# Performance work log

Measured on AMD Instinct MI355X. Metric: run time of the kernel, lower is better.

The kernel has to match this reference:

```python
import jax, jax.numpy as jnp
import numpy as np

N, E = 100000, 1000000          # nodes, edges
IN, OUT = 64, 64                # feature dims
R, B = 16, 8                    # num_rels, num_bases


def setup_inputs() -> dict:
    key = jax.random.key(0)
    k = jax.random.split(key, 6)
    h = jax.random.normal(k[0], (N, IN), jnp.float32)
    weight = jax.random.normal(k[1], (B, IN, OUT), jnp.float32) * 0.05
    w_comp = jax.random.normal(k[2], (R, B), jnp.float32) * 0.3
    src = jax.random.randint(k[3], (E,), 0, N, jnp.int32)
    dst = jax.random.randint(k[4], (E,), 0, N, jnp.int32)
    rel = jax.random.randint(k[5], (E,), 0, R, jnp.int32)
    return {"h": h, "weight": weight, "w_comp": w_comp,
            "src": src, "dst": dst, "rel": rel}


def _rel_weights(weight, w_comp):
    # Faithful replication of the torch basis-combination including its
    # exact (reinterpreting) view calls:
    #   weight.view(in, B, out); matmul(w_comp, .); .view(R, in, out)
    V = weight.reshape(IN, B, OUT)                 # reinterpret, not transpose
    M = jnp.einsum('rb,ibo->iro', w_comp, V)       # [IN, R, OUT]
    return M.reshape(R, IN, OUT)


def reference(h, weight, w_comp, src, dst, rel):
    W = _rel_weights(weight, w_comp)               # [R, IN, OUT]
    # msg_e = h[src_e] @ W[rel_e]; computed without materializing [E,IN,OUT]:
    proj = jnp.einsum('nd,rdf->nrf', h, W)         # [N, R, OUT]
    msg = proj[src, rel]                           # [E, OUT] per-edge gather
    h2 = jax.ops.segment_sum(msg, dst, num_segments=N)  # fn.sum -> 'h2'
    # apply_func: bias is None (falsy); returns activation(old h).
    # Note: original apply_func reads but does not use h2 (tutorial quirk);
    # we return both the updated 'h' and the aggregated 'h2'.
    h_new = jax.nn.relu(h)
    return h_new, h2
```

## Files before the change

kernel.cpp:

```cpp
#include <hip/hip_runtime.h>
#include <hip/hip_bf16.h>

#define NN 100000
#define EE 1000000
#define FDIM 64
#define NREL 16
#define NBASE 8
#define HN (NN * FDIM)
#define H4 (HN / 4)
#define WSZ (NREL * FDIM * FDIM)
#define NPAD 100032
#define PCOLS 1024
#define NB_SCAN ((NN + 255) / 256)
#define EGX 128

typedef __attribute__((ext_vector_type(8))) short short8;
typedef __attribute__((ext_vector_type(4))) float f32x4;

static __device__ __forceinline__ ushort f2bf(float f) {
    __hip_bfloat16 b = __float2bfloat16(f);
    return *(ushort*)&b;
}
static __device__ __forceinline__ float bf2f(ushort u) {
    unsigned x = ((unsigned)u) << 16;
    float f;
    __builtin_memcpy(&f, &x, 4);
    return f;
}

__global__ void prep_kernel(const float4* __restrict__ h4, float4* __restrict__ out4,
                            ushort2* __restrict__ hb2,
                            const float* __restrict__ weight,
                            const float* __restrict__ w_comp, ushort* __restrict__ WT,
                            int* __restrict__ cnt, int czn,
                            float4* __restrict__ h2z, int zero_h2) {
    int gid = blockIdx.x * blockDim.x + threadIdx.x;
    if (gid < czn) cnt[gid] = 0;
    if (gid < WSZ) {
        int r = gid >> 12;
        int o = (gid >> 6) & 63;
        int d = gid & 63;
        const float* wc = w_comp + (d & 15) * NBASE;
        const float* wv = weight + (size_t)(4 * r + (d >> 4)) * 512 + o;
        float acc = 0.f;
#pragma unroll
        for (int b = 0; b < NBASE; ++b)
            acc = fmaf(wc[b], wv[b * 64], acc);
        WT[gid] = f2bf(acc);
    }
    if (gid < H4) {
        float4 v = h4[gid];
        ushort2 lo, hi;
        lo.x = f2bf(v.x); lo.y = f2bf(v.y);
        hi.x = f2bf(v.z); hi.y = f2bf(v.w);
        hb2[2 * gid] = lo;
        hb2[2 * gid + 1] = hi;
        v.x = fmaxf(v.x, 0.f); v.y = fmaxf(v.y, 0.f);
        v.z = fmaxf(v.z, 0.f); v.w = fmaxf(v.w, 0.f);
        out4[gid] = v;
        if (zero_h2) h2z[gid] = make_float4(0.f, 0.f, 0.f, 0.f);
    }
}


__global__ __launch_bounds__(256) void proj_gemm_kernel(
    const ushort* __restrict__ hb, const ushort* __restrict__ WT,
    ushort* __restrict__ projb, const int* __restrict__ dst, int* __restrict__ cnt) {
    const int wv = threadIdx.x >> 6;
    const int lane = threadIdx.x & 63;
    const int quad = lane >> 4, l15 = lane & 15;
    const int row0 = blockIdx.x * 64;
    const int col0 = blockIdx.y * 256 + wv * 64;

    if (blockIdx.y == 0) {
        int tid = blockIdx.x * 256 + threadIdx.x;
        int stride = gridDim.x * 256;
        for (int i = tid; i < EE; i += stride)
            atomicAdd(&cnt[dst[i]], 1);
    }

    short8 Af[4][2];
#pragma unroll
    for (int g = 0; g < 4; ++g) {
        const short8* ar = (const short8*)(hb + (size_t)(row0 + 16 * g + l15) * 64);
        Af[g][0] = ar[quad];
        Af[g][1] = ar[4 + quad];
    }
    short8 Bf[2][4];
#pragma unroll
    for (int t = 0; t < 4; ++t) {
        const short8* br = (const short8*)(WT + (size_t)(col0 + 16 * t + l15) * 64);
        Bf[0][t] = br[quad];
        Bf[1][t] = br[4 + quad];
    }
    f32x4 acc[4][4];
#pragma unroll
    for (int g = 0; g < 4; ++g)
#pragma unroll
        for (int t = 0; t < 4; ++t) acc[g][t] = (f32x4){0.f, 0.f, 0.f, 0.f};
#pragma unroll
    for (int g = 0; g < 4; ++g)
#pragma unroll
        for (int t = 0; t < 4; ++t) {
            acc[g][t] = __builtin_amdgcn_mfma_f32_16x16x32_bf16(Af[g][0], Bf[0][t], acc[g][t], 0, 0, 0);
            acc[g][t] = __builtin_amdgcn_mfma_f32_16x16x32_bf16(Af[g][1], Bf[1][t], acc[g][t], 0, 0, 0);
        }
#pragma unroll
    for (int g = 0; g < 4; ++g) {
        int rbase = row0 + 16 * g + quad * 4;
#pragma unroll
        for (int t = 0; t < 4; ++t) {
            size_t cb = (size_t)(col0 + 16 * t + l15);
#pragma unroll
            for (int r = 0; r < 4; ++r)
                projb[(size_t)(rbase + r) * PCOLS + cb] = f2bf(acc[g][t][r]);
        }
    }
}

__global__ __launch_bounds__(256) void scan_a_kernel(const int* __restrict__ cnt,
                                                     int* __restrict__ bsum) {
    int i = blockIdx.x * 256 + threadIdx.x;
    int v = (i < NN) ? cnt[i] : 0;
#pragma unroll
    for (int o = 32; o > 0; o >>= 1) v += __shfl_down(v, o, 64);
    __shared__ int ws4[4];
    if ((threadIdx.x & 63) == 0) ws4[threadIdx.x >> 6] = v;
    __syncthreads();
    if (threadIdx.x == 0) bsum[blockIdx.x] = ws4[0] + ws4[1] + ws4[2] + ws4[3];
}

__global__ __launch_bounds__(512) void scan_b_kernel(const int* __restrict__ bsum,
                                                     int* __restrict__ bbase,
                                                     int* __restrict__ off) {
    __shared__ int lds[512];
    int t = threadIdx.x;
    int v = (t < NB_SCAN) ? bsum[t] : 0;
    lds[t] = v;
    __syncthreads();
    for (int o = 1; o < 512; o <<= 1) {
        int u = (t >= o) ? lds[t - o] : 0;
        __syncthreads();
        lds[t] += u;
        __syncthreads();
    }
    if (t < NB_SCAN) bbase[t] = lds[t] - v;
    if (t == NB_SCAN - 1) off[NN] = lds[t];
}

__global__ __launch_bounds__(256) void scan_c_kernel(const int* __restrict__ cnt,
                                                     const int* __restrict__ bbase,
                                                     int* __restrict__ off,
                                                     int* __restrict__ cur) {
    __shared__ int lds[256];
    int i = blockIdx.x * 256 + threadIdx.x;
    int t = threadIdx.x;
    int v = (i < NN) ? cnt[i] : 0;
    lds[t] = v;
    __syncthreads();
    for (int o = 1; o < 256; o <<= 1) {
        int u = (t >= o) ? lds[t - o] : 0;
        __syncthreads();
        lds[t] += u;
        __syncthreads();
    }
    if (i < NN) {
        int excl = lds[t] - v + bbase[blockIdx.x];
        off[i] = excl;
        cur[i] = excl;
    }
}

__global__ void scatter_dst_kernel(const int* __restrict__ src, const int* __restrict__ dst,
                                   const int* __restrict__ rel, int* __restrict__ cur,
                                   int* __restrict__ pidx) {
    int i = blockIdx.x * blockDim.x + threadIdx.x;
    if (i < EE) {
        int pos = atomicAdd(&cur[dst[i]], 1);
        pidx[pos] = src[i] * 16 + rel[i];
    }
}

__global__ __launch_bounds__(256) void aggregate_kernel(
    const int* __restrict__ off, const int* __restrict__ pidx,
    const ushort* __restrict__ projb, float* __restrict__ h2) {
    int wv = (blockIdx.x * 256 + threadIdx.x) >> 6;
    int lane = threadIdx.x & 63;
    int v = __builtin_amdgcn_readfirstlane(wv);
    if (v >= NN) return;
    int s = off[v], e = off[v + 1];
    float acc = 0.f;
    int i = s;
    for (; i + 4 <= e; i += 4) {
        int p0 = pidx[i], p1 = pidx[i + 1], p2 = pidx[i + 2], p3 = pidx[i + 3];
        float a = bf2f(projb[(size_t)p0 * 64 + lane]);
        float b = bf2f(projb[(size_t)p1 * 64 + lane]);
        float c = bf2f(projb[(size_t)p2 * 64 + lane]);
        float d = bf2f(projb[(size_t)p3 * 64 + lane]);
        acc += (a + b) + (c + d);
    }
    for (; i < e; ++i)
        acc += bf2f(projb[(size_t)pidx[i] * 64 + lane]);
    h2[(size_t)v * 64 + lane] = acc;
}


__global__ void hist16_kernel(const int* __restrict__ rel, int* __restrict__ counts) {
    __shared__ int lc[NREL];
    if (threadIdx.x < NREL) lc[threadIdx.x] = 0;
    __syncthreads();
    int stride = gridDim.x * blockDim.x;
    for (int i = blockIdx.x * blockDim.x + threadIdx.x; i < EE; i += stride)
        atomicAdd(&lc[rel[i]], 1);
    __syncthreads();
    if (threadIdx.x < NREL && lc[threadIdx.x] > 0)
        atomicAdd(&counts[threadIdx.x], lc[threadIdx.x]);
}

__global__ void scan16_kernel(const int* __restrict__ counts,
                              int* __restrict__ offsets, int* __restrict__ cursors) {
    if (threadIdx.x == 0 && blockIdx.x == 0) {
        int acc = 0;
        for (int r = 0; r < NREL; ++r) { offsets[r] = acc; cursors[r] = acc; acc += counts[r]; }
        offsets[NREL] = acc;
    }
}

__global__ void scatter16_kernel(const int* __restrict__ rel, const int* __restrict__ src,
                                 const int* __restrict__ dst, int* __restrict__ cursors,
                                 int* __restrict__ src_bin, int* __restrict__ dst_bin) {
    __shared__ int lhist[NREL];
    __shared__ int lbase[NREL];
    int i = blockIdx.x * blockDim.x + threadIdx.x;
    if (threadIdx.x < NREL) lhist[threadIdx.x] = 0;
    __syncthreads();
    int r = 0, rank = 0;
    if (i < EE) { r = rel[i]; rank = atomicAdd(&lhist[r], 1); }
    __syncthreads();
    if (threadIdx.x < NREL && lhist[threadIdx.x] > 0)
        lbase[threadIdx.x] = atomicAdd(&cursors[threadIdx.x], lhist[threadIdx.x]);
    __syncthreads();
    if (i < EE) {
        int pos = lbase[r] + rank;
        src_bin[pos] = src[i];
        dst_bin[pos] = dst[i];
    }
}

__global__ __launch_bounds__(256) void edge_mfma_kernel(
    const int* __restrict__ offsets, const int* __restrict__ src_bin,
    const int* __restrict__ dst_bin, const ushort* __restrict__ hb,
    const ushort* __restrict__ WT, float* __restrict__ h2) {
    const int rel = blockIdx.y;
    const int lane = threadIdx.x & 63;
    const int quad = lane >> 4;
    const int l15 = lane & 15;
    const int start = offsets[rel];
    const int end = offsets[rel + 1];
    const int cnt = end - start;
    if (cnt <= 0) return;

    const short8* wt = (const short8*)(WT + rel * 4096);
    short8 Bf[2][4];
#pragma unroll
    for (int t = 0; t < 4; ++t) {
#pragma unroll
        for (int s = 0; s < 2; ++s)
            Bf[s][t] = wt[((t * 16 + l15) << 3) + (s << 2) + quad];
    }
    const int nw = EGX * 4;
    const int wave = blockIdx.x * 4 + (threadIdx.x >> 6);
    const int nb = (cnt + 15) >> 4;
    const int per = (nb + nw - 1) / nw;
    int b0 = wave * per;
    int b1 = b0 + per; if (b1 > nb) b1 = nb;
    const int quad4 = quad * 4;

    for (int b = b0; b < b1; ++b) {
        const int base = start + (b << 4);
        int ei = base + l15; if (ei >= end) ei = end - 1;
        int s0 = src_bin[ei];
        const short8* ar = (const short8*)(hb + (size_t)s0 * FDIM);
        short8 A0 = ar[quad];
        short8 A1 = ar[4 + quad];
        f32x4 acc[4];
#pragma unroll
        for (int t = 0; t < 4; ++t) acc[t] = (f32x4){0.f, 0.f, 0.f, 0.f};
#pragma unroll
        for (int t = 0; t < 4; ++t) {
            acc[t] = __builtin_amdgcn_mfma_f32_16x16x32_bf16(A0, Bf[0][t], acc[t], 0, 0, 0);
            acc[t] = __builtin_amdgcn_mfma_f32_16x16x32_bf16(A1, Bf[1][t], acc[t], 0, 0, 0);
        }
#pragma unroll
        for (int r = 0; r < 4; ++r) {
            int em = base + quad4 + r;
            if (em < end) {
                int dv = dst_bin[em];
                float* p = h2 + (size_t)dv * FDIM + l15;
                unsafeAtomicAdd(p,      acc[0][r]);
                unsafeAtomicAdd(p + 16, acc[1][r]);
                unsafeAtomicAdd(p + 32, acc[2][r]);
                unsafeAtomicAdd(p + 48, acc[3][r]);
            }
        }
    }
}

extern "C" void kernel_launch(void* const* d_in, const int* in_sizes, int n_in,
                              void* d_out, int out_size, void* d_ws, size_t ws_size,
                              hipStream_t stream) {
    const float* h      = (const float*)d_in[0];
    const float* weight = (const float*)d_in[1];
    const float* w_comp = (const float*)d_in[2];
    const int*   src    = (const int*)d_in[3];
    const int*   dst    = (const int*)d_in[4];
    const int*   rel    = (const int*)d_in[5];

    float* out_hnew = (float*)d_out;
    float* out_h2   = out_hnew + HN;

    char* ws = (char*)d_ws;

    size_t o_cnt  = 131072;
    size_t o_off  = o_cnt + 400000;
    size_t o_cur  = o_off + 400016;
    size_t o_pidx = o_cur + 400000;
    size_t o_bsum = o_pidx + 4000000;
    size_t o_bbas = o_bsum + 4 * ((NB_SCAN + 3) & ~3);
    size_t o_hb   = o_bbas + 4 * ((NB_SCAN + 3) & ~3);
    size_t o_proj = o_hb + (size_t)NPAD * 128;
    size_t need   = o_proj + (size_t)NPAD * 2048;

    if (ws_size >= need) {
        ushort* WT    = (ushort*)ws;
        int*    cnt   = (int*)(ws + o_cnt);
        int*    off   = (int*)(ws + o_off);
        int*    cur   = (int*)(ws + o_cur);
        int*    pidx  = (int*)(ws + o_pidx);
        int*    bsum  = (int*)(ws + o_bsum);
        int*    bbase = (int*)(ws + o_bbas);
        ushort* hb    = (ushort*)(ws + o_hb);
        ushort* projb = (ushort*)(ws + o_proj);

        hipLaunchKernelGGL(prep_kernel, dim3((H4 + 255) / 256), dim3(256), 0, stream,
                           (const float4*)h, (float4*)out_hnew, (ushort2*)hb,
                           weight, w_comp, WT, cnt, NN, (float4*)out_h2, 0);
        hipLaunchKernelGGL(proj_gemm_kernel, dim3(NPAD / 64, 4), dim3(256), 0, stream,
                           hb, WT, projb, dst, cnt);
        hipLaunchKernelGGL(scan_a_kernel, dim3(NB_SCAN), dim3(256), 0, stream, cnt, bsum);
        hipLaunchKernelGGL(scan_b_kernel, dim3(1), dim3(512), 0, stream, bsum, bbase, off);
        hipLaunchKernelGGL(scan_c_kernel, dim3(NB_SCAN), dim3(256), 0, stream,
                           cnt, bbase, off, cur);
        hipLaunchKernelGGL(scatter_dst_kernel, dim3((EE + 255) / 256), dim3(256), 0, stream,
                           src, dst, rel, cur, pidx);
        hipLaunchKernelGGL(aggregate_kernel, dim3(NN / 4), dim3(256), 0, stream,
                           off, pidx, projb, out_h2);
    } else {
        ushort* WT      = (ushort*)ws;
        int*    meta    = (int*)(ws + 0x20000);
        int*    counts  = meta;
        int*    offsets = meta + 16;
        int*    cursors = meta + 33;
        int*    src_bin = (int*)(ws + 0x20400);
        int*    dst_bin = (int*)(ws + 0x20400 + 4 * EE);
        ushort* hb      = (ushort*)(ws + 0x20400 + 8 * EE);

        hipLaunchKernelGGL(prep_kernel, dim3((H4 + 255) / 256), dim3(256), 0, stream,
                           (const float4*)h, (float4*)out_hnew, (ushort2*)hb,
                           weight, w_comp, WT, counts, 16, (float4*)out_h2, 1);
        hipLaunchKernelGGL(hist16_kernel, dim3(1024), dim3(256), 0, stream, rel, counts);
        hipLaunchKernelGGL(scan16_kernel, dim3(1), dim3(64), 0, stream,
                           counts, offsets, cursors);
        hipLaunchKernelGGL(scatter16_kernel, dim3((EE + 255) / 256), dim3(256), 0, stream,
                           rel, src, dst, cursors, src_bin, dst_bin);
        hipLaunchKernelGGL(edge_mfma_kernel, dim3(EGX, NREL), dim3(256), 0, stream,
                           offsets, src_bin, dst_bin, hb, WT, out_h2);
    }
}
```

Baseline: 324.3 us.

## Fuse scan stages and scatter+aggregate into persistent kernels with grid barriers

```diff
diff --git a/kernel.cpp b/kernel.cpp
--- a/kernel.cpp
+++ b/kernel.cpp
@@ -11,7 +11,9 @@
 #define WSZ (NREL * FDIM * FDIM)
 #define NPAD 100032
 #define PCOLS 1024
-#define NB_SCAN ((NN + 255) / 256)
+#define SB 512
+#define NBLK ((NN + SB - 1) / SB)
+#define SAB 512
 #define EGX 128
 
 typedef __attribute__((ext_vector_type(8))) short short8;
@@ -79,129 +81,148 @@
             atomicAdd(&cnt[dst[i]], 1);
     }
 
-    short8 Af[4][2];
+    short8 Wf[4][2];
+#pragma unroll
+    for (int ct = 0; ct < 4; ++ct) {
+        const short8* wr = (const short8*)(WT + (size_t)(col0 + 16 * ct + l15) * 64);
+        Wf[ct][0] = wr[quad];
+        Wf[ct][1] = wr[4 + quad];
+    }
+    short8 Hf[4][2];
 #pragma unroll
     for (int g = 0; g < 4; ++g) {
-        const short8* ar = (const short8*)(hb + (size_t)(row0 + 16 * g + l15) * 64);
-        Af[g][0] = ar[quad];
-        Af[g][1] = ar[4 + quad];
-    }
-    short8 Bf[2][4];
-#pragma unroll
-    for (int t = 0; t < 4; ++t) {
-        const short8* br = (const short8*)(WT + (size_t)(col0 + 16 * t + l15) * 64);
-        Bf[0][t] = br[quad];
-        Bf[1][t] = br[4 + quad];
+        const short8* hr = (const short8*)(hb + (size_t)(row0 + 16 * g + l15) * 64);
+        Hf[g][0] = hr[quad];
+        Hf[g][1] = hr[4 + quad];
     }
     f32x4 acc[4][4];
 #pragma unroll
-    for (int g = 0; g < 4; ++g)
-#pragma unroll
-        for (int t = 0; t < 4; ++t) acc[g][t] = (f32x4){0.f, 0.f, 0.f, 0.f};
-#pragma unroll
-    for (int g = 0; g < 4; ++g)
-#pragma unroll
-        for (int t = 0; t < 4; ++t) {
-            acc[g][t] = __builtin_amdgcn_mfma_f32_16x16x32_bf16(Af[g][0], Bf[0][t], acc[g][t], 0, 0, 0);
-            acc[g][t] = __builtin_amdgcn_mfma_f32_16x16x32_bf16(Af[g][1], Bf[1][t], acc[g][t], 0, 0, 0);
+    for (int ct = 0; ct < 4; ++ct)
+#pragma unroll
+        for (int g = 0; g < 4; ++g) acc[ct][g] = (f32x4){0.f, 0.f, 0.f, 0.f};
+#pragma unroll
+    for (int ct = 0; ct < 4; ++ct)
+#pragma unroll
+        for (int g = 0; g < 4; ++g) {
+            acc[ct][g] = __builtin_amdgcn_mfma_f32_16x16x32_bf16(Wf[ct][0], Hf[g][0], acc[ct][g], 0, 0, 0);
+            acc[ct][g] = __builtin_amdgcn_mfma_f32_16x16x32_bf16(Wf[ct][1], Hf[g][1], acc[ct][g], 0, 0, 0);
         }
 #pragma unroll
     for (int g = 0; g < 4; ++g) {
-        int rbase = row0 + 16 * g + quad * 4;
-#pragma unroll
-        for (int t = 0; t < 4; ++t) {
-            size_t cb = (size_t)(col0 + 16 * t + l15);
-#pragma unroll
-            for (int r = 0; r < 4; ++r)
-                projb[(size_t)(rbase + r) * PCOLS + cb] = f2bf(acc[g][t][r]);
-        }
-    }
-}
-
-__global__ __launch_bounds__(256) void scan_a_kernel(const int* __restrict__ cnt,
-                                                     int* __restrict__ bsum) {
-    int i = blockIdx.x * 256 + threadIdx.x;
+        size_t nrow = (size_t)(row0 + 16 * g + l15) * PCOLS;
+#pragma unroll
+        for (int ct = 0; ct < 4; ++ct) {
+            int c = col0 + 16 * ct + quad * 4;
+            unsigned u0 = ((unsigned)f2bf(acc[ct][g][1]) << 16) | f2bf(acc[ct][g][0]);
+            unsigned u1 = ((unsigned)f2bf(acc[ct][g][3]) << 16) | f2bf(acc[ct][g][2]);
+            *(uint2*)(projb + nrow + c) = make_uint2(u0, u1);
+        }
+    }
+}
+
+__global__ __launch_bounds__(SB) void scan_fused_kernel(
+    const int* __restrict__ cnt, int* __restrict__ off, int* __restrict__ cur,
+    int* __restrict__ bsum, int* __restrict__ bbase, int* __restrict__ sync) {
+    __shared__ int lds[SB];
+    __shared__ int lastBlk;
+    const int b = blockIdx.x, t = threadIdx.x;
+    const int i = b * SB + t;
     int v = (i < NN) ? cnt[i] : 0;
-#pragma unroll
-    for (int o = 32; o > 0; o >>= 1) v += __shfl_down(v, o, 64);
-    __shared__ int ws4[4];
-    if ((threadIdx.x & 63) == 0) ws4[threadIdx.x >> 6] = v;
-    __syncthreads();
-    if (threadIdx.x == 0) bsum[blockIdx.x] = ws4[0] + ws4[1] + ws4[2] + ws4[3];
-}
-
-__global__ __launch_bounds__(512) void scan_b_kernel(const int* __restrict__ bsum,
-                                                     int* __restrict__ bbase,
-                                                     int* __restrict__ off) {
-    __shared__ int lds[512];
-    int t = threadIdx.x;
-    int v = (t < NB_SCAN) ? bsum[t] : 0;
     lds[t] = v;
     __syncthreads();
-    for (int o = 1; o < 512; o <<= 1) {
+    for (int o = 1; o < SB; o <<= 1) {
         int u = (t >= o) ? lds[t - o] : 0;
         __syncthreads();
         lds[t] += u;
         __syncthreads();
     }
-    if (t < NB_SCAN) bbase[t] = lds[t] - v;
-    if (t == NB_SCAN - 1) off[NN] = lds[t];
-}
-
-__global__ __launch_bounds__(256) void scan_c_kernel(const int* __restrict__ cnt,
-                                                     const int* __restrict__ bbase,
-                                                     int* __restrict__ off,
-                                                     int* __restrict__ cur) {
-    __shared__ int lds[256];
-    int i = blockIdx.x * 256 + threadIdx.x;
-    int t = threadIdx.x;
-    int v = (i < NN) ? cnt[i] : 0;
-    lds[t] = v;
-    __syncthreads();
-    for (int o = 1; o < 256; o <<= 1) {
-        int u = (t >= o) ? lds[t - o] : 0;
+    int incl = lds[t];
+    if (t == SB - 1) bsum[b] = incl;
+    __threadfence();
+    __syncthreads();
+    if (t == 0) {
+        int prev = __hip_atomic_fetch_add(&sync[0], 1, __ATOMIC_ACQ_REL, __HIP_MEMORY_SCOPE_AGENT);
+        lastBlk = (prev == gridDim.x - 1);
+    }
+    __syncthreads();
+    if (lastBlk) {
+        __shared__ int lds2[256];
+        int vb = 0;
+        if (t < 256) {
+            vb = (t < NBLK) ? __hip_atomic_load(&bsum[t], __ATOMIC_RELAXED, __HIP_MEMORY_SCOPE_AGENT) : 0;
+            lds2[t] = vb;
+        }
         __syncthreads();
-        lds[t] += u;
+        for (int o = 1; o < 256; o <<= 1) {
+            int u = (t >= o && t < 256) ? lds2[t - o] : 0;
+            __syncthreads();
+            if (t < 256) lds2[t] += u;
+            __syncthreads();
+        }
+        if (t < NBLK) bbase[t] = lds2[t] - vb;
+        if (t == NBLK - 1) off[NN] = lds2[t];
+        __threadfence();
         __syncthreads();
-    }
+        if (t == 0)
+            __hip_atomic_store(&sync[1], 1, __ATOMIC_RELEASE, __HIP_MEMORY_SCOPE_AGENT);
+    }
+    if (t == 0) {
+        while (__hip_atomic_load(&sync[1], __ATOMIC_ACQUIRE, __HIP_MEMORY_SCOPE_AGENT) == 0)
+            __builtin_amdgcn_s_sleep(8);
+    }
+    __syncthreads();
+    int base = __hip_atomic_load(&bbase[b], __ATOMIC_RELAXED, __HIP_MEMORY_SCOPE_AGENT);
     if (i < NN) {
-        int excl = lds[t] - v + bbase[blockIdx.x];
+        int excl = incl - v + base;
         off[i] = excl;
         cur[i] = excl;
     }
 }
 
-__global__ void scatter_dst_kernel(const int* __restrict__ src, const int* __restrict__ dst,
-                                   const int* __restrict__ rel, int* __restrict__ cur,
-                                   int* __restrict__ pidx) {
-    int i = blockIdx.x * blockDim.x + threadIdx.x;
-    if (i < EE) {
+__global__ __launch_bounds__(256) void scatter_agg_kernel(
+    const int* __restrict__ src, const int* __restrict__ dst,
+    const int* __restrict__ rel, int* __restrict__ cur, int* __restrict__ pidx,
+    const int* __restrict__ off, const ushort* __restrict__ projb,
+    float* __restrict__ h2, int* __restrict__ sync) {
+    int tid = blockIdx.x * 256 + threadIdx.x;
+    int stride = SAB * 256;
+    for (int i = tid; i < EE; i += stride) {
         int pos = atomicAdd(&cur[dst[i]], 1);
         pidx[pos] = src[i] * 16 + rel[i];
     }
-}
-
-__global__ __launch_bounds__(256) void aggregate_kernel(
-    const int* __restrict__ off, const int* __restrict__ pidx,
-    const ushort* __restrict__ projb, float* __restrict__ h2) {
-    int wv = (blockIdx.x * 256 + threadIdx.x) >> 6;
-    int lane = threadIdx.x & 63;
-    int v = __builtin_amdgcn_readfirstlane(wv);
-    if (v >= NN) return;
-    int s = off[v], e = off[v + 1];
-    float acc = 0.f;
-    int i = s;
-    for (; i + 4 <= e; i += 4) {
-        int p0 = pidx[i], p1 = pidx[i + 1], p2 = pidx[i + 2], p3 = pidx[i + 3];
-        float a = bf2f(projb[(size_t)p0 * 64 + lane]);
-        float b = bf2f(projb[(size_t)p1 * 64 + lane]);
-        float c = bf2f(projb[(size_t)p2 * 64 + lane]);
-        float d = bf2f(projb[(size_t)p3 * 64 + lane]);
-        acc += (a + b) + (c + d);
-    }
-    for (; i < e; ++i)
-        acc += bf2f(projb[(size_t)pidx[i] * 64 + lane]);
-    h2[(size_t)v * 64 + lane] = acc;
+    __threadfence();
+    __syncthreads();
+    if (threadIdx.x == 0) {
+        __hip_atomic_fetch_add(&sync[2], 1, __ATOMIC_ACQ_REL, __HIP_MEMORY_SCOPE_AGENT);
+        while (__hip_atomic_load(&sync[2], __ATOMIC_ACQUIRE, __HIP_MEMORY_SCOPE_AGENT) < SAB)
+            __builtin_amdgcn_s_sleep(8);
+    }
+    __syncthreads();
+
+    const int lane = threadIdx.x & 63;
+    const int w = tid >> 6;
+    const int nwv = SAB * 4;
+    for (int v = w; v < NN; v += nwv) {
+        int s = off[v], e = off[v + 1];
+        float acc = 0.f;
+        int i = s;
+        for (; i + 4 <= e; i += 4) {
+            int p0 = __hip_atomic_load(&pidx[i],     __ATOMIC_RELAXED, __HIP_MEMORY_SCOPE_AGENT);
+            int p1 = __hip_atomic_load(&pidx[i + 1], __ATOMIC_RELAXED, __HIP_MEMORY_SCOPE_AGENT);
+            int p2 = __hip_atomic_load(&pidx[i + 2], __ATOMIC_RELAXED, __HIP_MEMORY_SCOPE_AGENT);
+            int p3 = __hip_atomic_load(&pidx[i + 3], __ATOMIC_RELAXED, __HIP_MEMORY_SCOPE_AGENT);
+            float a = bf2f(projb[(size_t)p0 * 64 + lane]);
+            float b = bf2f(projb[(size_t)p1 * 64 + lane]);
+            float c = bf2f(projb[(size_t)p2 * 64 + lane]);
+            float d = bf2f(projb[(size_t)p3 * 64 + lane]);
+            acc += (a + b) + (c + d);
+        }
+        for (; i < e; ++i) {
+            int p = __hip_atomic_load(&pidx[i], __ATOMIC_RELAXED, __HIP_MEMORY_SCOPE_AGENT);
+            acc += bf2f(projb[(size_t)p * 64 + lane]);
+        }
+        h2[(size_t)v * 64 + lane] = acc;
+    }
 }
 
 
@@ -322,18 +343,19 @@
     char* ws = (char*)d_ws;
 
     size_t o_cnt  = 131072;
-    size_t o_off  = o_cnt + 400000;
+    size_t o_off  = o_cnt + 400032;
     size_t o_cur  = o_off + 400016;
     size_t o_pidx = o_cur + 400000;
     size_t o_bsum = o_pidx + 4000000;
-    size_t o_bbas = o_bsum + 4 * ((NB_SCAN + 3) & ~3);
-    size_t o_hb   = o_bbas + 4 * ((NB_SCAN + 3) & ~3);
+    size_t o_bbas = o_bsum + 4 * ((NBLK + 3) & ~3);
+    size_t o_hb   = o_bbas + 4 * ((NBLK + 3) & ~3);
     size_t o_proj = o_hb + (size_t)NPAD * 128;
     size_t need   = o_proj + (size_t)NPAD * 2048;
 
     if (ws_size >= need) {
         ushort* WT    = (ushort*)ws;
         int*    cnt   = (int*)(ws + o_cnt);
+        int*    sync  = cnt + NN;
         int*    off   = (int*)(ws + o_off);
         int*    cur   = (int*)(ws + o_cur);
         int*    pidx  = (int*)(ws + o_pidx);
@@ -344,17 +366,13 @@
 
         hipLaunchKernelGGL(prep_kernel, dim3((H4 + 255) / 256), dim3(256), 0, stream,
                            (const float4*)h, (float4*)out_hnew, (ushort2*)hb,
-                           weight, w_comp, WT, cnt, NN, (float4*)out_h2, 0);
+                           weight, w_comp, WT, cnt, NN + 4, (float4*)out_h2, 0);
         hipLaunchKernelGGL(proj_gemm_kernel, dim3(NPAD / 64, 4), dim3(256), 0, stream,
                            hb, WT, projb, dst, cnt);
-        hipLaunchKernelGGL(scan_a_kernel, dim3(NB_SCAN), dim3(256), 0, stream, cnt, bsum);
-        hipLaunchKernelGGL(scan_b_kernel, dim3(1), dim3(512), 0, stream, bsum, bbase, off);
-        hipLaunchKernelGGL(scan_c_kernel, dim3(NB_SCAN), dim3(256), 0, stream,
-                           cnt, bbase, off, cur);
-        hipLaunchKernelGGL(scatter_dst_kernel, dim3((EE + 255) / 256), dim3(256), 0, stream,
-                           src, dst, rel, cur, pidx);
-        hipLaunchKernelGGL(aggregate_kernel, dim3(NN / 4), dim3(256), 0, stream,
-                           off, pidx, projb, out_h2);
+        hipLaunchKernelGGL(scan_fused_kernel, dim3(NBLK), dim3(SB), 0, stream,
+                           cnt, off, cur, bsum, bbase, sync);
+        hipLaunchKernelGGL(scatter_agg_kernel, dim3(SAB), dim3(256), 0, stream,
+                           src, dst, rel, cur, pidx, off, projb, out_h2, sync);
     } else {
         ushort* WT      = (ushort*)ws;
         int*    meta    = (int*)(ws + 0x20000);
```

Measured after the change: 589.8 us. 1.82x slower.
